# Performance work log

Measured on AMD Instinct MI355X. Metric: run time of the kernel, lower is better.

Reference implementation:

```python
import jax, jax.numpy as jnp
import numpy as np

K = 20          # knn neighbors (hard-coded default in source)
BN_EPS = 1e-3   # keras BatchNormalization default epsilon


def setup_inputs() -> dict:
    key = jax.random.key(0)
    ks = jax.random.split(key, 8)
    B, N, D = 8, 4096, 64
    x = jax.random.normal(ks[0], (B, N, D), dtype=jnp.float32)
    # Conv1D(kernel_size=1) == pointwise dense over feature dim
    w1 = jax.random.normal(ks[1], (2 * D, 32), dtype=jnp.float32) * 0.05
    b1 = jnp.zeros((32,), dtype=jnp.float32)
    g1 = jnp.ones((32,), dtype=jnp.float32)
    be1 = jnp.zeros((32,), dtype=jnp.float32)
    w2 = jax.random.normal(ks[2], (32, 64), dtype=jnp.float32) * 0.05
    b2 = jnp.zeros((64,), dtype=jnp.float32)
    g2 = jnp.ones((64,), dtype=jnp.float32)
    be2 = jnp.zeros((64,), dtype=jnp.float32)
    wd = jax.random.normal(ks[3], (64, N), dtype=jnp.float32) * 0.05
    bd = jnp.zeros((N,), dtype=jnp.float32)
    return {"x": x, "w1": w1, "b1": b1, "g1": g1, "be1": be1,
            "w2": w2, "b2": b2, "g2": g2, "be2": be2, "wd": wd, "bd": bd}


def _batchnorm(h, gamma, beta):
    # batch-stat normalization over (batch, points) axes, like BN(momentum=0) in training
    mean = jnp.mean(h, axis=(0, 1), keepdims=True)
    var = jnp.var(h, axis=(0, 1), keepdims=True)
    return gamma * (h - mean) * jax.lax.rsqrt(var + BN_EPS) + beta


def reference(x, w1, b1, g1, be1, w2, b2, g2, be2, wd, bd):
    B, N, D = x.shape
    # pairwise squared L2 distance: ||a||^2 - 2 a.b + ||b||^2  -> (B, N, N)
    inner = jnp.einsum('bnd,bmd->bnm', x, x)
    sq = jnp.sum(jnp.square(x), axis=-1, keepdims=True)  # (B, N, 1)
    adj = sq - 2.0 * inner + jnp.swapaxes(sq, 1, 2)
    # KNN: top-k of negative distance
    _, knn_idx = jax.lax.top_k(-adj, K)                   # (B, N, K)
    # gather neighbor features (B, N, K, D)
    neighbors = jax.vmap(lambda xf, idx: xf[idx])(x, knn_idx)
    central = x[:, :, None, :]                            # (B, N, 1, D)
    edge = jnp.concatenate(
        [jnp.broadcast_to(central, (B, N, K, D)), neighbors - central], axis=-1)
    feat = jnp.max(edge, axis=2)                          # (B, N, 2D)
    h = jax.nn.relu(feat @ w1 + b1)
    h = _batchnorm(h, g1, be1)
    h = jax.nn.relu(h @ w2 + b2)
    h = _batchnorm(h, g2, be2)
    pooled = jnp.max(h, axis=1)                           # (B, 64)
    return jax.nn.softmax(pooled @ wd + bd, axis=-1)      # (B, N)
```

## Files before the change

kernel.cpp:

```cpp
#include <hip/hip_runtime.h>
#include <stdint.h>

#define N_PTS 4096
#define B_SZ 8
#define D_DIM 64
#define KNN 20
#define NROWS (B_SZ * N_PTS)
#define H1C 32
#define H2C 64
#define BN_EPS 1e-3f
#define NSLICE 2
#define SLICE_C (N_PTS / NSLICE)
#define NT (SLICE_C / 64)

typedef __attribute__((ext_vector_type(8))) short bf16x8;
typedef __attribute__((ext_vector_type(4))) float f32x4;
typedef unsigned long long ull;

__device__ __forceinline__ ushort f2bf(float f) {
    uint32_t u = __float_as_uint(f);
    uint32_t r = (u + 0x7fffu + ((u >> 16) & 1u)) >> 16;
    return (ushort)r;
}
__device__ __forceinline__ float bf2f(ushort h) {
    return __uint_as_float(((uint32_t)h) << 16);
}

__device__ __forceinline__ void ins20(ull (&k)[KNN], ull cur) {
#pragma unroll
    for (int p = KNN - 1; p >= 1; --p) {
        bool c = cur < k[p - 1];
        ull t = (k[p] < cur) ? k[p] : cur;
        k[p] = c ? k[p - 1] : t;
    }
    k[0] = (k[0] < cur) ? k[0] : cur;
}

__device__ __forceinline__ void ce_asc(ull& a, ull& b) {
    bool c = b < a;
    ull lo = c ? b : a;
    ull hi = c ? a : b;
    a = lo;
    b = hi;
}

__device__ __forceinline__ void merge8(ull (&k)[KNN], ull (&e)[8]) {
    ce_asc(e[0], e[1]); ce_asc(e[2], e[3]); ce_asc(e[4], e[5]); ce_asc(e[6], e[7]);
    ce_asc(e[0], e[2]); ce_asc(e[1], e[3]); ce_asc(e[4], e[6]); ce_asc(e[5], e[7]);
    ce_asc(e[1], e[2]); ce_asc(e[5], e[6]);
    ce_asc(e[0], e[4]); ce_asc(e[1], e[5]); ce_asc(e[2], e[6]); ce_asc(e[3], e[7]);
    ce_asc(e[2], e[4]); ce_asc(e[3], e[5]);
    ce_asc(e[1], e[2]); ce_asc(e[3], e[4]); ce_asc(e[5], e[6]);
    ull u[12];
    u[0] = k[16]; u[1] = k[17]; u[2] = k[18]; u[3] = k[19];
#pragma unroll
    for (int j = 0; j < 8; ++j) {
        ull a = k[8 + j], b = e[7 - j];
        bool c = b < a;
        k[8 + j] = c ? b : a;
        ull hi = c ? a : b;
        if (j < 4) u[8 + j] = hi;
        else       u[j]     = hi;
    }
#pragma unroll
    for (int j = 0; j < 8; ++j) ce_asc(k[j], k[j + 8]);
#pragma unroll
    for (int j = 0; j < 4; ++j) { ce_asc(k[j], k[j + 4]); ce_asc(k[8 + j], k[12 + j]); }
#pragma unroll
    for (int j = 0; j < 2; ++j) {
        ce_asc(k[j], k[j + 2]);       ce_asc(k[4 + j], k[6 + j]);
        ce_asc(k[8 + j], k[10 + j]);  ce_asc(k[12 + j], k[14 + j]);
    }
#pragma unroll
    for (int j = 0; j < 16; j += 2) ce_asc(k[j], k[j + 1]);
#pragma unroll
    for (int j = 0; j < 4; ++j) ce_asc(u[j], u[j + 8]);
#pragma unroll
    for (int j = 0; j < 4; ++j) ce_asc(u[j], u[j + 4]);
    ce_asc(u[0], u[2]); ce_asc(u[1], u[3]);
    ce_asc(u[0], u[1]); ce_asc(u[2], u[3]);
    k[16] = u[0]; k[17] = u[1]; k[18] = u[2]; k[19] = u[3];
}

__global__ void prep_kernel(const float* __restrict__ x, ushort* __restrict__ xh,
                            ushort* __restrict__ xl, float* __restrict__ sq) {
    int row = blockIdx.x * blockDim.x + threadIdx.x;
    if (row >= NROWS) return;
    const float4* xr = (const float4*)(x + (size_t)row * D_DIM);
    ushort4* ho = (ushort4*)(xh + (size_t)row * D_DIM);
    ushort4* lo = (ushort4*)(xl + (size_t)row * D_DIM);
    float acc = 0.f;
#pragma unroll
    for (int q = 0; q < 16; ++q) {
        float4 v = xr[q];
        acc = fmaf(v.x, v.x, acc);
        acc = fmaf(v.y, v.y, acc);
        acc = fmaf(v.z, v.z, acc);
        acc = fmaf(v.w, v.w, acc);
        ushort4 h, l;
        h.x = f2bf(v.x); l.x = f2bf(v.x - bf2f(h.x));
        h.y = f2bf(v.y); l.y = f2bf(v.y - bf2f(h.y));
        h.z = f2bf(v.z); l.z = f2bf(v.z - bf2f(h.z));
        h.w = f2bf(v.w); l.w = f2bf(v.w - bf2f(h.w));
        ho[q] = h; lo[q] = l;
    }
    sq[row] = acc;
}

__global__ __launch_bounds__(256, 4) void dist_topk(
    const ushort* __restrict__ xh, const ushort* __restrict__ xl,
    const float* __restrict__ sq, ull* __restrict__ part) {
    int tid = threadIdx.x;
    int lane = tid & 63;
    int w = tid >> 6;
    int b = blockIdx.x & 7;
    int blk = blockIdx.x >> 3;
    int slice = blockIdx.y;
    const ushort* xhb = xh + (size_t)b * N_PTS * D_DIM;
    const ushort* xlb = xl + (size_t)b * N_PTS * D_DIM;
    const float* sqb = sq + (size_t)b * N_PTS;

    int qr0 = blk * 64 + w * 16;
    int fr = lane & 15;
    int fg = lane >> 4;

    bf16x8 q_h[2], q_l[2];
    {
        const ushort* ph = xhb + (size_t)(qr0 + fr) * D_DIM + fg * 8;
        const ushort* pl = xlb + (size_t)(qr0 + fr) * D_DIM + fg * 8;
        q_h[0] = *(const bf16x8*)(ph);
        q_h[1] = *(const bf16x8*)(ph + 32);
        q_l[0] = *(const bf16x8*)(pl);
        q_l[1] = *(const bf16x8*)(pl + 32);
    }
    float sqi = sqb[qr0 + fr];

    ull k20[KNN];
#pragma unroll
    for (int p = 0; p < KNN; ++p) k20[p] = ~0ull;
    ull e[8];
#pragma unroll
    for (int i = 0; i < 8; ++i) e[i] = ~0ull;
    int cnt = 0;
    unsigned thr = 0xFFFFFFFFu;

    int cbase = slice * SLICE_C;
    const ushort* pah = xhb + (size_t)(cbase + fr) * D_DIM + fg * 8;
    const ushort* pal = xlb + (size_t)(cbase + fr) * D_DIM + fg * 8;
    const float* psq = sqb + cbase + fg * 4;

    for (int t = 0; t < NT; ++t) {
        int c0 = cbase + t * 64;
#pragma unroll
        for (int s = 0; s < 4; ++s) {
            int cc = c0 + s * 16;
            bf16x8 a_h0 = *(const bf16x8*)(pah + s * 16 * D_DIM);
            bf16x8 a_h1 = *(const bf16x8*)(pah + s * 16 * D_DIM + 32);
            bf16x8 a_l0 = *(const bf16x8*)(pal + s * 16 * D_DIM);
            bf16x8 a_l1 = *(const bf16x8*)(pal + s * 16 * D_DIM + 32);
            float4 sqj = *(const float4*)(psq + s * 16);
            f32x4 accA = {0.f, 0.f, 0.f, 0.f};
            f32x4 accB = {0.f, 0.f, 0.f, 0.f};
            accA = __builtin_amdgcn_mfma_f32_16x16x32_bf16(a_h0, q_h[0], accA, 0, 0, 0);
            accB = __builtin_amdgcn_mfma_f32_16x16x32_bf16(a_h0, q_l[0], accB, 0, 0, 0);
            accA = __builtin_amdgcn_mfma_f32_16x16x32_bf16(a_h1, q_h[1], accA, 0, 0, 0);
            accB = __builtin_amdgcn_mfma_f32_16x16x32_bf16(a_h1, q_l[1], accB, 0, 0, 0);
            accB = __builtin_amdgcn_mfma_f32_16x16x32_bf16(a_l0, q_h[0], accB, 0, 0, 0);
            accB = __builtin_amdgcn_mfma_f32_16x16x32_bf16(a_l1, q_h[1], accB, 0, 0, 0);
            float sqjv[4] = {sqj.x, sqj.y, sqj.z, sqj.w};
#pragma unroll
            for (int qq = 0; qq < 4; ++qq) {
                float base = sqi + sqjv[qq];
                float d = fmaf(-2.f, accA[qq], fmaf(-2.f, accB[qq], base));
                d = fmaxf(d, 0.f);
                unsigned u = __float_as_uint(d);
                if (u <= thr) {
                    e[7] = e[6]; e[6] = e[5]; e[5] = e[4]; e[4] = e[3];
                    e[3] = e[2]; e[2] = e[1]; e[1] = e[0];
                    e[0] = (((ull)u) << 32) | (unsigned)(cc + fg * 4 + qq);
                    ++cnt;
                }
            }
            if (__any(cnt >= 5)) {
                merge8(k20, e);
#pragma unroll
                for (int i = 0; i < 8; ++i) e[i] = ~0ull;
                cnt = 0;
                unsigned t5  = (unsigned)(k20[4]  >> 32);
                unsigned t20 = (unsigned)(k20[19] >> 32);
                unsigned o;
                o = __shfl_xor(t5, 16);  t5  = (o > t5)  ? o : t5;
                o = __shfl_xor(t5, 32);  t5  = (o > t5)  ? o : t5;
                o = __shfl_xor(t20, 16); t20 = (o < t20) ? o : t20;
                o = __shfl_xor(t20, 32); t20 = (o < t20) ? o : t20;
                thr = (t5 < t20) ? t5 : t20;
            }
        }
        pah += 64 * D_DIM;
        pal += 64 * D_DIM;
        psq += 64;
    }
    if (__any(cnt >= 1)) {
        merge8(k20, e);
    }

#pragma unroll
    for (int g = 1; g < 4; ++g) {
        for (int p = 0; p < KNN; ++p) {
            ull key = __shfl(k20[p], fr + 16 * g);
            bool useful = (lane < 16) && (key < k20[KNN - 1]);
            if (!__any(useful ? 1 : 0)) break;
            if (lane < 16) ins20(k20, key);
        }
    }
    if (lane < 16) {
        int grow = b * N_PTS + blk * 64 + w * 16 + lane;
#pragma unroll
        for (int p = 0; p < KNN; ++p)
            part[((size_t)(slice * KNN + p)) * NROWS + grow] = k20[p];
    }
}

__global__ void knn_merge(const ull* __restrict__ part, int* __restrict__ knn) {
    int row = blockIdx.x * blockDim.x + threadIdx.x;
    if (row >= NROWS) return;
    ull fin[KNN];
#pragma unroll
    for (int p = 0; p < KNN; ++p) fin[p] = part[(size_t)p * NROWS + row];
    for (int sl = 1; sl < NSLICE; ++sl) {
        for (int p = 0; p < KNN; ++p) {
            ull key = part[(size_t)(sl * KNN + p) * NROWS + row];
            if (key >= fin[KNN - 1]) break;
            ins20(fin, key);
        }
    }
#pragma unroll
    for (int q = 0; q < KNN; ++q)
        knn[(size_t)q * NROWS + row] = (int)(unsigned)(fin[q] & 0xffffffffu);
}

__global__ void edge_mlp1(const float* __restrict__ x, const int* __restrict__ knn,
                          const float* __restrict__ w1, const float* __restrict__ b1,
                          float* __restrict__ h1) {
    __shared__ float w1t[H1C][132];
    __shared__ float feat[4][128];
    int tid = threadIdx.x;
    int wave = tid >> 6, lane = tid & 63;
    for (int idx = tid; idx < 128 * H1C; idx += 256) {
        int f = idx >> 5, c = idx & 31;
        w1t[c][f] = w1[idx];
    }
    int row = blockIdx.x * 4 + wave;
    int b = row >> 12;
    int n = row & (N_PTS - 1);
    const float* xb = x + (size_t)b * N_PTS * D_DIM;
    float central = xb[(size_t)n * D_DIM + lane];
    float m = -1e30f;
    for (int k = 0; k < KNN; ++k) {
        int j = knn[(size_t)k * NROWS + row];
        float xn = xb[(size_t)j * D_DIM + lane];
        m = fmaxf(m, xn - central);
    }
    feat[wave][lane] = central;
    feat[wave][64 + lane] = m;
    __syncthreads();
    if (lane < H1C) {
        int c = lane;
        float acc = b1[c];
#pragma unroll
        for (int fq = 0; fq < 32; ++fq) {
            float4 fv = *(const float4*)(&feat[wave][fq * 4]);
            float4 wv = *(const float4*)(&w1t[c][fq * 4]);
            acc = fmaf(fv.x, wv.x, acc);
            acc = fmaf(fv.y, wv.y, acc);
            acc = fmaf(fv.z, wv.z, acc);
            acc = fmaf(fv.w, wv.w, acc);
        }
        h1[(size_t)row * H1C + c] = fmaxf(acc, 0.f);
    }
}

template <int CH>
__global__ void stats_kernel(const float* __restrict__ h, float* __restrict__ sum,
                             float* __restrict__ sumsq) {
    const int RPI = 256 / CH;
    int tid = threadIdx.x;
    int c = tid % CH;
    int r0 = tid / CH;
    float s = 0.f, s2 = 0.f;
    for (int r = blockIdx.x * RPI + r0; r < NROWS; r += gridDim.x * RPI) {
        float v = h[(size_t)r * CH + c];
        s += v;
        s2 = fmaf(v, v, s2);
    }
    __shared__ float ls[256], ls2[256];
    ls[tid] = s; ls2[tid] = s2;
    __syncthreads();
    for (int step = 128; step >= CH; step >>= 1) {
        if (tid < step) { ls[tid] += ls[tid + step]; ls2[tid] += ls2[tid + step]; }
        __syncthreads();
    }
    if (tid < CH) {
        atomicAdd(&sum[tid], ls[tid]);
        atomicAdd(&sumsq[tid], ls2[tid]);
    }
}

template <int CH>
__global__ void coeff_kernel(const float* sum, const float* sumsq, const float* g,
                             const float* be, float* a, float* cc) {
    int c = threadIdx.x;
    if (c >= CH) return;
    float mean = sum[c] * (1.f / NROWS);
    float var = sumsq[c] * (1.f / NROWS) - mean * mean;
    float aa = g[c] * rsqrtf(var + BN_EPS);
    a[c] = aa;
    cc[c] = be[c] - aa * mean;
}

__global__ void mlp2_kernel(const float* __restrict__ h1, const float* __restrict__ w2,
                            const float* __restrict__ b2, const float* __restrict__ a1,
                            const float* __restrict__ c1, float* __restrict__ h2) {
    __shared__ float w2s[H1C][H2C];
    __shared__ float hb[4][H1C];
    int tid = threadIdx.x;
    for (int idx = tid; idx < H1C * H2C; idx += 256)
        w2s[idx >> 6][idx & 63] = w2[idx];
    int rw = tid >> 6;
    int c = tid & 63;
    int row = blockIdx.x * 4 + rw;
    if (c < H1C) {
        float v = h1[(size_t)row * H1C + c];
        hb[rw][c] = fmaf(a1[c], v, c1[c]);
    }
    __syncthreads();
    float acc = b2[c];
#pragma unroll
    for (int f = 0; f < H1C; ++f)
        acc = fmaf(hb[rw][f], w2s[f][c], acc);
    h2[(size_t)row * H2C + c] = fmaxf(acc, 0.f);
}

__global__ void pool_part(const float* __restrict__ h2, float* __restrict__ pmax,
                          float* __restrict__ pmin) {
    int bb = blockIdx.x >> 6;
    int ch = blockIdx.x & 63;
    int tid = threadIdx.x;
    int rw = tid >> 6, c = tid & 63;
    float mx = -1e30f, mn = 1e30f;
    const float* hbase = h2 + (size_t)bb * N_PTS * H2C;
    for (int n = ch * 64 + rw; n < (ch + 1) * 64; n += 4) {
        float v = hbase[(size_t)n * H2C + c];
        mx = fmaxf(mx, v);
        mn = fminf(mn, v);
    }
    __shared__ float smx[256], smn[256];
    smx[tid] = mx; smn[tid] = mn;
    __syncthreads();
    if (tid < 128) { smx[tid] = fmaxf(smx[tid], smx[tid + 128]); smn[tid] = fminf(smn[tid], smn[tid + 128]); }
    __syncthreads();
    if (tid < 64) {
        pmax[((size_t)bb * 64 + ch) * 64 + tid] = fmaxf(smx[tid], smx[tid + 64]);
        pmin[((size_t)bb * 64 + ch) * 64 + tid] = fminf(smn[tid], smn[tid + 64]);
    }
}

__global__ void pool_final(const float* pmax, const float* pmin, const float* a2,
                           const float* c2, float* pooled) {
    int bb = blockIdx.x;
    int c = threadIdx.x;
    float M = -1e30f, m = 1e30f;
    for (int ch = 0; ch < 64; ++ch) {
        M = fmaxf(M, pmax[((size_t)bb * 64 + ch) * 64 + c]);
        m = fminf(m, pmin[((size_t)bb * 64 + ch) * 64 + c]);
    }
    float aa = a2[c];
    pooled[bb * 64 + c] = (aa >= 0.f) ? fmaf(aa, M, c2[c]) : fmaf(aa, m, c2[c]);
}

__global__ __launch_bounds__(256) void logits_kernel(const float* __restrict__ pooled,
                                                     const float* __restrict__ wd,
                                                     const float* __restrict__ bd,
                                                     float* __restrict__ lg) {
    __shared__ float pl[8][64];
    int tid = threadIdx.x;
    for (int i = tid; i < 8 * 64; i += 256) ((float*)pl)[i] = pooled[i];
    __syncthreads();
    int col = blockIdx.x * 64 + (tid & 63);
    int bg = tid >> 6;
    float acc0 = bd[col];
    float acc1 = acc0;
#pragma unroll
    for (int c = 0; c < 64; ++c) {
        float wv = wd[(size_t)c * N_PTS + col];
        acc0 = fmaf(pl[bg][c], wv, acc0);
        acc1 = fmaf(pl[bg + 4][c], wv, acc1);
    }
    lg[(size_t)bg * N_PTS + col] = acc0;
    lg[(size_t)(bg + 4) * N_PTS + col] = acc1;
}

__global__ __launch_bounds__(1024) void softmax_kernel(const float* __restrict__ lg,
                                                       float* __restrict__ out) {
    int bb = blockIdx.x;
    int tid = threadIdx.x;
    __shared__ float red[1024];
    float logit[4];
#pragma unroll
    for (int q = 0; q < 4; ++q)
        logit[q] = lg[(size_t)bb * N_PTS + tid + q * 1024];
    float mx = fmaxf(fmaxf(logit[0], logit[1]), fmaxf(logit[2], logit[3]));
    red[tid] = mx;
    __syncthreads();
    for (int s = 512; s >= 1; s >>= 1) {
        if (tid < s) red[tid] = fmaxf(red[tid], red[tid + s]);
        __syncthreads();
    }
    float gmax = red[0];
    __syncthreads();
    float e[4];
    float ssum = 0.f;
#pragma unroll
    for (int q = 0; q < 4; ++q) { e[q] = __expf(logit[q] - gmax); ssum += e[q]; }
    red[tid] = ssum;
    __syncthreads();
    for (int s = 512; s >= 1; s >>= 1) {
        if (tid < s) red[tid] += red[tid + s];
        __syncthreads();
    }
    float inv = 1.f / red[0];
#pragma unroll
    for (int q = 0; q < 4; ++q)
        out[(size_t)bb * N_PTS + tid + q * 1024] = e[q] * inv;
}

extern "C" void kernel_launch(void* const* d_in, const int* in_sizes, int n_in,
                              void* d_out, int out_size, void* d_ws, size_t ws_size,
                              hipStream_t stream) {
    (void)in_sizes; (void)n_in; (void)out_size; (void)ws_size;
    const float* x   = (const float*)d_in[0];
    const float* w1  = (const float*)d_in[1];
    const float* b1  = (const float*)d_in[2];
    const float* g1  = (const float*)d_in[3];
    const float* be1 = (const float*)d_in[4];
    const float* w2  = (const float*)d_in[5];
    const float* b2  = (const float*)d_in[6];
    const float* g2  = (const float*)d_in[7];
    const float* be2 = (const float*)d_in[8];
    const float* wd  = (const float*)d_in[9];
    const float* bd  = (const float*)d_in[10];

    char* ws = (char*)d_ws;
    size_t off = 0;
    auto alloc = [&](size_t bytes) -> void* {
        void* p = ws + off;
        off += (bytes + 255) & ~(size_t)255;
        return p;
    };
    ushort* xh = (ushort*)alloc((size_t)NROWS * D_DIM * 2);
    ushort* xl = (ushort*)alloc((size_t)NROWS * D_DIM * 2);
    float* sq = (float*)alloc((size_t)NROWS * 4);
    ull* part = (ull*)alloc((size_t)NROWS * NSLICE * KNN * 8);
    int* knn = (int*)alloc((size_t)NROWS * KNN * 4);
    float* h1 = (float*)alloc((size_t)NROWS * H1C * 4);
    float* h2 = (float*)alloc((size_t)NROWS * H2C * 4);
    float* stats = (float*)alloc(4096);
    float* pmax = (float*)alloc(8 * 64 * 64 * 4);
    float* pmin = (float*)alloc(8 * 64 * 64 * 4);
    float* pooled = (float*)alloc(8 * 64 * 4);
    float* lg = (float*)alloc((size_t)B_SZ * N_PTS * 4);

    float* sum1 = stats,       *sumsq1 = stats + 32, *a1 = stats + 64,  *c1 = stats + 96;
    float* sum2 = stats + 128, *sumsq2 = stats + 192, *a2 = stats + 256, *c2 = stats + 320;

    hipMemsetAsync(stats, 0, 4096, stream);

    prep_kernel<<<NROWS / 256, 256, 0, stream>>>(x, xh, xl, sq);
    dist_topk<<<dim3(B_SZ * 64, NSLICE), 256, 0, stream>>>(xh, xl, sq, part);
    knn_merge<<<NROWS / 256, 256, 0, stream>>>(part, knn);
    edge_mlp1<<<NROWS / 4, 256, 0, stream>>>(x, knn, w1, b1, h1);
    stats_kernel<H1C><<<256, 256, 0, stream>>>(h1, sum1, sumsq1);
    coeff_kernel<H1C><<<1, 32, 0, stream>>>(sum1, sumsq1, g1, be1, a1, c1);
    mlp2_kernel<<<NROWS / 4, 256, 0, stream>>>(h1, w2, b2, a1, c1, h2);
    stats_kernel<H2C><<<256, 256, 0, stream>>>(h2, sum2, sumsq2);
    coeff_kernel<H2C><<<1, 64, 0, stream>>>(sum2, sumsq2, g2, be2, a2, c2);
    pool_part<<<512, 256, 0, stream>>>(h2, pmax, pmin);
    pool_final<<<8, 64, 0, stream>>>(pmax, pmin, a2, c2, pooled);
    logits_kernel<<<64, 256, 0, stream>>>(pooled, wd, bd, lg);
    softmax_kernel<<<8, 1024, 0, stream>>>(lg, (float*)d_out);
}
```

Before: 414.0 us.

## Software-prefetch dist_topk candidate loads and fold BN coefficient kernels into consumers

The distance/top-k loop is flattened into a single loop over 16-column sub-tiles. It register-prefetches the next tile's bf16 hi/lo rows and squared norms while the current tile's MFMAs and selection run, aiming to hide global load latency. Separately, the two tiny coeff_kernel launches are removed and the BN scale and shift are recomputed inline in mlp2_kernel and pool_final, saving two launches. The cost is extra registers for the prefetch buffers and redundant per-thread coefficient math.

Measured after the change: 454.1 us. +9.7%, slower.

```diff
diff --git a/kernel.cpp b/kernel.cpp
--- a/kernel.cpp
+++ b/kernel.cpp
@@ -11,7 +11,7 @@
 #define BN_EPS 1e-3f
 #define NSLICE 2
 #define SLICE_C (N_PTS / NSLICE)
-#define NT (SLICE_C / 64)
+#define NSUB (SLICE_C / 16)
 
 typedef __attribute__((ext_vector_type(8))) short bf16x8;
 typedef __attribute__((ext_vector_type(4))) float f32x4;
@@ -149,56 +149,62 @@
     const ushort* pal = xlb + (size_t)(cbase + fr) * D_DIM + fg * 8;
     const float* psq = sqb + cbase + fg * 4;
 
-    for (int t = 0; t < NT; ++t) {
-        int c0 = cbase + t * 64;
-#pragma unroll
-        for (int s = 0; s < 4; ++s) {
-            int cc = c0 + s * 16;
-            bf16x8 a_h0 = *(const bf16x8*)(pah + s * 16 * D_DIM);
-            bf16x8 a_h1 = *(const bf16x8*)(pah + s * 16 * D_DIM + 32);
-            bf16x8 a_l0 = *(const bf16x8*)(pal + s * 16 * D_DIM);
-            bf16x8 a_l1 = *(const bf16x8*)(pal + s * 16 * D_DIM + 32);
-            float4 sqj = *(const float4*)(psq + s * 16);
-            f32x4 accA = {0.f, 0.f, 0.f, 0.f};
-            f32x4 accB = {0.f, 0.f, 0.f, 0.f};
-            accA = __builtin_amdgcn_mfma_f32_16x16x32_bf16(a_h0, q_h[0], accA, 0, 0, 0);
-            accB = __builtin_amdgcn_mfma_f32_16x16x32_bf16(a_h0, q_l[0], accB, 0, 0, 0);
-            accA = __builtin_amdgcn_mfma_f32_16x16x32_bf16(a_h1, q_h[1], accA, 0, 0, 0);
-            accB = __builtin_amdgcn_mfma_f32_16x16x32_bf16(a_h1, q_l[1], accB, 0, 0, 0);
-            accB = __builtin_amdgcn_mfma_f32_16x16x32_bf16(a_l0, q_h[0], accB, 0, 0, 0);
-            accB = __builtin_amdgcn_mfma_f32_16x16x32_bf16(a_l1, q_h[1], accB, 0, 0, 0);
-            float sqjv[4] = {sqj.x, sqj.y, sqj.z, sqj.w};
-#pragma unroll
-            for (int qq = 0; qq < 4; ++qq) {
-                float base = sqi + sqjv[qq];
-                float d = fmaf(-2.f, accA[qq], fmaf(-2.f, accB[qq], base));
-                d = fmaxf(d, 0.f);
-                unsigned u = __float_as_uint(d);
-                if (u <= thr) {
-                    e[7] = e[6]; e[6] = e[5]; e[5] = e[4]; e[4] = e[3];
-                    e[3] = e[2]; e[2] = e[1]; e[1] = e[0];
-                    e[0] = (((ull)u) << 32) | (unsigned)(cc + fg * 4 + qq);
-                    ++cnt;
-                }
-            }
-            if (__any(cnt >= 5)) {
-                merge8(k20, e);
-#pragma unroll
-                for (int i = 0; i < 8; ++i) e[i] = ~0ull;
-                cnt = 0;
-                unsigned t5  = (unsigned)(k20[4]  >> 32);
-                unsigned t20 = (unsigned)(k20[19] >> 32);
-                unsigned o;
-                o = __shfl_xor(t5, 16);  t5  = (o > t5)  ? o : t5;
-                o = __shfl_xor(t5, 32);  t5  = (o > t5)  ? o : t5;
-                o = __shfl_xor(t20, 16); t20 = (o < t20) ? o : t20;
-                o = __shfl_xor(t20, 32); t20 = (o < t20) ? o : t20;
-                thr = (t5 < t20) ? t5 : t20;
+    bf16x8 n_h0 = *(const bf16x8*)(pah);
+    bf16x8 n_h1 = *(const bf16x8*)(pah + 32);
+    bf16x8 n_l0 = *(const bf16x8*)(pal);
+    bf16x8 n_l1 = *(const bf16x8*)(pal + 32);
+    float4 n_sq = *(const float4*)(psq);
+
+#pragma unroll 4
+    for (int i = 0; i < NSUB; ++i) {
+        bf16x8 a_h0 = n_h0, a_h1 = n_h1, a_l0 = n_l0, a_l1 = n_l1;
+        float4 sqj = n_sq;
+        int adv = (i == NSUB - 1) ? 0 : 16 * D_DIM;
+        int advq = (i == NSUB - 1) ? 0 : 16;
+        pah += adv; pal += adv; psq += advq;
+        n_h0 = *(const bf16x8*)(pah);
+        n_h1 = *(const bf16x8*)(pah + 32);
+        n_l0 = *(const bf16x8*)(pal);
+        n_l1 = *(const bf16x8*)(pal + 32);
+        n_sq = *(const float4*)(psq);
+
+        int cc = cbase + i * 16;
+        f32x4 accA = {0.f, 0.f, 0.f, 0.f};
+        f32x4 accB = {0.f, 0.f, 0.f, 0.f};
+        accA = __builtin_amdgcn_mfma_f32_16x16x32_bf16(a_h0, q_h[0], accA, 0, 0, 0);
+        accB = __builtin_amdgcn_mfma_f32_16x16x32_bf16(a_h0, q_l[0], accB, 0, 0, 0);
+        accA = __builtin_amdgcn_mfma_f32_16x16x32_bf16(a_h1, q_h[1], accA, 0, 0, 0);
+        accB = __builtin_amdgcn_mfma_f32_16x16x32_bf16(a_h1, q_l[1], accB, 0, 0, 0);
+        accB = __builtin_amdgcn_mfma_f32_16x16x32_bf16(a_l0, q_h[0], accB, 0, 0, 0);
+        accB = __builtin_amdgcn_mfma_f32_16x16x32_bf16(a_l1, q_h[1], accB, 0, 0, 0);
+        float sqjv[4] = {sqj.x, sqj.y, sqj.z, sqj.w};
+#pragma unroll
+        for (int qq = 0; qq < 4; ++qq) {
+            float base = sqi + sqjv[qq];
+            float d = fmaf(-2.f, accA[qq], fmaf(-2.f, accB[qq], base));
+            d = fmaxf(d, 0.f);
+            unsigned u = __float_as_uint(d);
+            if (u <= thr) {
+                e[7] = e[6]; e[6] = e[5]; e[5] = e[4]; e[4] = e[3];
+                e[3] = e[2]; e[2] = e[1]; e[1] = e[0];
+                e[0] = (((ull)u) << 32) | (unsigned)(cc + fg * 4 + qq);
+                ++cnt;
             }
         }
-        pah += 64 * D_DIM;
-        pal += 64 * D_DIM;
-        psq += 64;
+        if (__any(cnt >= 5)) {
+            merge8(k20, e);
+#pragma unroll
+            for (int j = 0; j < 8; ++j) e[j] = ~0ull;
+            cnt = 0;
+            unsigned t5  = (unsigned)(k20[4]  >> 32);
+            unsigned t20 = (unsigned)(k20[19] >> 32);
+            unsigned o;
+            o = __shfl_xor(t5, 16);  t5  = (o > t5)  ? o : t5;
+            o = __shfl_xor(t5, 32);  t5  = (o > t5)  ? o : t5;
+            o = __shfl_xor(t20, 16); t20 = (o < t20) ? o : t20;
+            o = __shfl_xor(t20, 32); t20 = (o < t20) ? o : t20;
+            thr = (t5 < t20) ? t5 : t20;
+        }
     }
     if (__any(cnt >= 1)) {
         merge8(k20, e);
@@ -306,21 +312,10 @@
     }
 }
 
-template <int CH>
-__global__ void coeff_kernel(const float* sum, const float* sumsq, const float* g,
-                             const float* be, float* a, float* cc) {
-    int c = threadIdx.x;
-    if (c >= CH) return;
-    float mean = sum[c] * (1.f / NROWS);
-    float var = sumsq[c] * (1.f / NROWS) - mean * mean;
-    float aa = g[c] * rsqrtf(var + BN_EPS);
-    a[c] = aa;
-    cc[c] = be[c] - aa * mean;
-}
-
 __global__ void mlp2_kernel(const float* __restrict__ h1, const float* __restrict__ w2,
-                            const float* __restrict__ b2, const float* __restrict__ a1,
-                            const float* __restrict__ c1, float* __restrict__ h2) {
+                            const float* __restrict__ b2, const float* __restrict__ sum1,
+                            const float* __restrict__ sumsq1, const float* __restrict__ g1,
+                            const float* __restrict__ be1, float* __restrict__ h2) {
     __shared__ float w2s[H1C][H2C];
     __shared__ float hb[4][H1C];
     int tid = threadIdx.x;
@@ -330,8 +325,12 @@
     int c = tid & 63;
     int row = blockIdx.x * 4 + rw;
     if (c < H1C) {
+        float mean = sum1[c] * (1.f / NROWS);
+        float var = sumsq1[c] * (1.f / NROWS) - mean * mean;
+        float aa = g1[c] * rsqrtf(var + BN_EPS);
+        float ccf = be1[c] - aa * mean;
         float v = h1[(size_t)row * H1C + c];
-        hb[rw][c] = fmaf(a1[c], v, c1[c]);
+        hb[rw][c] = fmaf(aa, v, ccf);
     }
     __syncthreads();
     float acc = b2[c];
@@ -365,8 +364,10 @@
     }
 }
 
-__global__ void pool_final(const float* pmax, const float* pmin, const float* a2,
-                           const float* c2, float* pooled) {
+__global__ void pool_final(const float* pmax, const float* pmin,
+                           const float* __restrict__ sum2, const float* __restrict__ sumsq2,
+                           const float* __restrict__ g2, const float* __restrict__ be2,
+                           float* pooled) {
     int bb = blockIdx.x;
     int c = threadIdx.x;
     float M = -1e30f, m = 1e30f;
@@ -374,8 +375,11 @@
         M = fmaxf(M, pmax[((size_t)bb * 64 + ch) * 64 + c]);
         m = fminf(m, pmin[((size_t)bb * 64 + ch) * 64 + c]);
     }
-    float aa = a2[c];
-    pooled[bb * 64 + c] = (aa >= 0.f) ? fmaf(aa, M, c2[c]) : fmaf(aa, m, c2[c]);
+    float mean = sum2[c] * (1.f / NROWS);
+    float var = sumsq2[c] * (1.f / NROWS) - mean * mean;
+    float aa = g2[c] * rsqrtf(var + BN_EPS);
+    float ccf = be2[c] - aa * mean;
+    pooled[bb * 64 + c] = (aa >= 0.f) ? fmaf(aa, M, ccf) : fmaf(aa, m, ccf);
 }
 
 __global__ __launch_bounds__(256) void logits_kernel(const float* __restrict__ pooled,
@@ -470,8 +474,8 @@
     float* pooled = (float*)alloc(8 * 64 * 4);
     float* lg = (float*)alloc((size_t)B_SZ * N_PTS * 4);
 
-    float* sum1 = stats,       *sumsq1 = stats + 32, *a1 = stats + 64,  *c1 = stats + 96;
-    float* sum2 = stats + 128, *sumsq2 = stats + 192, *a2 = stats + 256, *c2 = stats + 320;
+    float* sum1 = stats,       *sumsq1 = stats + 32;
+    float* sum2 = stats + 128, *sumsq2 = stats + 192;
 
     hipMemsetAsync(stats, 0, 4096, stream);
 
@@ -480,12 +484,10 @@
     knn_merge<<<NROWS / 256, 256, 0, stream>>>(part, knn);
     edge_mlp1<<<NROWS / 4, 256, 0, stream>>>(x, knn, w1, b1, h1);
     stats_kernel<H1C><<<256, 256, 0, stream>>>(h1, sum1, sumsq1);
-    coeff_kernel<H1C><<<1, 32, 0, stream>>>(sum1, sumsq1, g1, be1, a1, c1);
-    mlp2_kernel<<<NROWS / 4, 256, 0, stream>>>(h1, w2, b2, a1, c1, h2);
+    mlp2_kernel<<<NROWS / 4, 256, 0, stream>>>(h1, w2, b2, sum1, sumsq1, g1, be1, h2);
     stats_kernel<H2C><<<256, 256, 0, stream>>>(h2, sum2, sumsq2);
-    coeff_kernel<H2C><<<1, 64, 0, stream>>>(sum2, sumsq2, g2, be2, a2, c2);
     pool_part<<<512, 256, 0, stream>>>(h2, pmax, pmin);
-    pool_final<<<8, 64, 0, stream>>>(pmax, pmin, a2, c2, pooled);
+    pool_final<<<8, 64, 0, stream>>>(pmax, pmin, sum2, sumsq2, g2, be2, pooled);
     logits_kernel<<<64, 256, 0, stream>>>(pooled, wd, bd, lg);
     softmax_kernel<<<8, 1024, 0, stream>>>(lg, (float*)d_out);
 }
```
